# Kernel tuning notes

Measured on AMD Instinct MI355X. Metric: run time of the kernel, lower is better.

Reference implementation:

```python
import jax, jax.numpy as jnp
import numpy as np
from jax import lax

TH = 1.0      # float threshold from __init__
TAU = 0.1     # forward default
EPS_BN = 1e-5
EPS_NORM = 1e-8


def setup_inputs() -> dict:
    key = jax.random.key(0)
    ks = jax.random.split(key, 9)
    B, C, T, N = 1, 256, 128, 256
    HID = 32
    return {
        'v_rel': jax.random.normal(ks[0], (B, C, T, N), jnp.float32),
        'w1': jax.random.normal(ks[1], (HID, 2), jnp.float32) * 0.05,
        'b1': jax.random.normal(ks[2], (HID,), jnp.float32) * 0.05,
        'bn_gamma': jax.random.uniform(ks[3], (HID,), jnp.float32) + 0.5,
        'bn_beta': jax.random.normal(ks[4], (HID,), jnp.float32) * 0.05,
        'bn_mean': jax.random.normal(ks[5], (HID,), jnp.float32) * 0.05,
        'bn_var': jax.random.uniform(ks[6], (HID,), jnp.float32) + 0.5,
        'w2': jax.random.normal(ks[7], (1, HID), jnp.float32) * 0.05,
        'b2': jax.random.normal(ks[8], (1,), jnp.float32) * 0.05,
    }


def _per_ch(p):
    return p[None, :, None, None]


def _dist_mat(v_rel, w1, b1, bn_gamma, bn_beta, bn_mean, bn_var, w2, b2):
    # d_type == 'learned': pairwise diffs of last-frame absolute features (first 2 channels)
    x = v_rel[:, :2, -1, :]                       # (1, 2, N)
    d = x[:, :, :, None] - x[:, :, None, :]       # (1, 2, N, N) == reshaped temp
    h = jnp.einsum('oi,binm->bonm', w1, d) + _per_ch(b1)   # 1x1 conv -> (1, HID, N, N)
    h = jax.nn.relu(h)
    # BatchNorm2d, inference mode with running stats
    h = (h - _per_ch(bn_mean)) * (_per_ch(bn_gamma) / jnp.sqrt(_per_ch(bn_var) + EPS_BN)) + _per_ch(bn_beta)
    h = jnp.exp(jnp.einsum('oi,binm->bonm', w2, h) + _per_ch(b2))  # (1, 1, N, N)
    dm = 0.5 * (h + jnp.swapaxes(h, -1, -2))      # mean of stack(temp, temp^T)
    return dm[:, 0].mean(axis=0)                  # squeeze(1).mean(dim=0) -> (N, N)


def _find_group_indices(dist, th):
    # Serial union-find over strictly-lower-triangular close pairs in row-major
    # order, exactly matching the torch loop semantics; expressed as lax.scan.
    N = dist.shape[0]
    flat = jnp.arange(N * N)
    r = flat // N
    c = flat % N
    ok = (c < r) & (dist[r, c] <= th)

    def step(labels, inp):
        ri, ci, o = inp
        merged = jnp.where(labels == labels[ri], labels[ci], labels)
        return jnp.where(o, merged, labels), None

    labels, _ = lax.scan(step, jnp.arange(N), (r, c, ok))
    # relabel sorted-unique labels to 0..K-1 (labels are in [0, N))
    present = jnp.zeros(N, jnp.int32).at[labels].set(1)
    ranks = jnp.cumsum(present) - 1
    return ranks[labels]


def reference(v_rel, w1, b1, bn_gamma, bn_beta, bn_mean, bn_var, w2, b2):
    B, C, T, N = v_rel.shape
    dm = _dist_mat(v_rel, w1, b1, bn_gamma, bn_beta, bn_mean, bn_var, w2, b2)  # (N, N)
    group_indices = _find_group_indices(dm, TH)[None]                          # (1, N)
    # group_backprop_trick with tau=0.1, hard=True (straight-through)
    sig = jax.nn.sigmoid(-(dm - TH) / TAU)
    sig_norm = sig / (sig.sum(axis=0, keepdims=True) + EPS_NORM)
    v = v_rel[0]                                                               # (C, T, N)
    v_soft = jnp.einsum('ctn,nm->ctm', v, sig_norm)
    v_grouped = (lax.stop_gradient(v - v_soft) + v_soft)[None]                 # (1, C, T, N)
    dist_mat_full = jnp.broadcast_to(dm[None, None], (B, T, N, N))
    return v_grouped, group_indices, dist_mat_full
```

## Files before the change

### kernel.cpp

```cpp
#include <hip/hip_runtime.h>
#include <stdint.h>

#define NN 256
#define TT 128
#define CC 256
#define TH_F 1.0f
#define EPS_BN_F 1e-5f

#define OUT0_ELEMS (CC * TT * NN)
#define OUT1_OFF   OUT0_ELEMS
#define OUT2_OFF   (OUT0_ELEMS + NN)

#define N0_F4      (OUT0_ELEMS / 4)
#define NSLICE_F4  (NN * NN / 4)
#define F4_PER_BLK 1024
#define COPY0_BLKS (N0_F4 / F4_PER_BLK)
#define COPY2_BLKS (((TT - 1) * NSLICE_F4) / F4_PER_BLK)

typedef float vfloat4 __attribute__((ext_vector_type(4)));

__global__ __launch_bounds__(256) void k1_dm_out0(
        const float* __restrict__ v_rel,
        const float* __restrict__ w1,
        const float* __restrict__ b1,
        const float* __restrict__ bn_g,
        const float* __restrict__ bn_b,
        const float* __restrict__ bn_m,
        const float* __restrict__ bn_v,
        const float* __restrict__ w2,
        const float* __restrict__ b2,
        float* __restrict__ out) {
    const int tid = threadIdx.x;
    if (blockIdx.x < NN) {
        float* __restrict__ dm = out + OUT2_OFF;
        const int m = tid;
        const int n = blockIdx.x;
        const float x0n = v_rel[127 * 256 + n];
        const float x0m = v_rel[127 * 256 + m];
        const float x1n = v_rel[255 * 256 + n];
        const float x1m = v_rel[255 * 256 + m];
        const float d0 = x0n - x0m;
        const float d1 = x1n - x1m;
        float accF = 0.0f, accB = 0.0f;
        #pragma unroll
        for (int o = 0; o < 32; ++o) {
            const float w10 = w1[2 * o], w11 = w1[2 * o + 1];
            const float scale = bn_g[o] / sqrtf(bn_v[o] + EPS_BN_F);
            const float mu = bn_m[o], be = bn_b[o], bb = b1[o], a = w2[o];
            float preF = w10 * d0 + w11 * d1 + bb;
            float preB = w10 * (-d0) + w11 * (-d1) + bb;
            float hF = fmaxf(preF, 0.0f);
            float hB = fmaxf(preB, 0.0f);
            accF += a * ((hF - mu) * scale + be);
            accB += a * ((hB - mu) * scale + be);
        }
        const float sF = expf(accF + b2[0]);
        const float sB = expf(accB + b2[0]);
        dm[n * 256 + m] = 0.5f * (sF + sB);
    } else {
        const int base = (int)(blockIdx.x - NN) * F4_PER_BLK + tid;
        const vfloat4* __restrict__ in4 = reinterpret_cast<const vfloat4*>(v_rel);
        vfloat4* __restrict__ o0 = reinterpret_cast<vfloat4*>(out);
        #pragma unroll
        for (int q = 0; q < 4; ++q) {
            const int i = base + q * 256;
            __builtin_nontemporal_store(in4[i], o0 + i);
        }
    }
}

__device__ __forceinline__ uint32_t rl32(uint32_t v, uint32_t l) {
    return (uint32_t)__builtin_amdgcn_readlane((int)v, (int)l);
}
__device__ __forceinline__ uint64_t rl64(uint64_t v, uint32_t l) {
    uint32_t lo = rl32((uint32_t)v, l);
    uint32_t hi = rl32((uint32_t)(v >> 32), l);
    return ((uint64_t)hi << 32) | lo;
}

template<int NW>
__device__ __forceinline__ uint32_t pick_lab(uint32_t lab0, uint32_t lab1,
                                             uint32_t lab2, uint32_t lab3,
                                             uint32_t p) {
    const uint32_t ls = p & 63u;
    uint32_t a = rl32(lab0, ls);
    if (NW == 1) return a;
    uint32_t b = rl32(lab1, ls);
    const uint32_t g = (p >> 6) & 3u;
    if (NW == 2) return (g & 1u) ? b : a;
    uint32_t c = rl32(lab2, ls);
    uint32_t d = (NW > 3) ? rl32(lab3, ls) : c;
    uint32_t ab = (g & 1u) ? b : a;
    uint32_t cd = (g & 1u) ? d : c;
    return (g & 2u) ? cd : ab;
}

template<int NW>
__device__ __forceinline__ void scan_chunk(const int K, const int lane,
                                           uint32_t& lab0, uint32_t& lab1,
                                           uint32_t& lab2, uint32_t& lab3,
                                           uint32_t& labw,
                                           const uint64_t* __restrict__ bits,
                                           bool& fast, uint32_t& V) {
    const int base = (K * 64 + lane) * 4;
    uint64_t Wr0 = bits[base + 0];
    uint64_t Wr1 = (NW > 1) ? bits[base + 1] : 0;
    uint64_t Wr2 = (NW > 2) ? bits[base + 2] : 0;
    uint64_t Wr3 = (NW > 3) ? bits[base + 3] : 0;

    const uint64_t rowOr = Wr0 | Wr1 | Wr2 | Wr3;
    const uint64_t nonempty = __ballot(rowOr != 0);

    if (fast && nonempty == ~0ull) {
        labw = V;
        return;
    }

    for (int rr = 0; rr < 64; ++rr) {
        const bool rowEmpty = ((nonempty >> rr) & 1ull) == 0ull;
        if (fast) {
            if (!rowEmpty) {
                labw = ((uint32_t)lane == (uint32_t)rr) ? V : labw;
                continue;
            }
            fast = (V == (uint32_t)(K * 64 + rr));
            continue;
        }
        const uint64_t w0 = rl64(Wr0, (uint32_t)rr);
        const uint64_t w1 = (NW > 1) ? rl64(Wr1, (uint32_t)rr) : 0;
        const uint64_t w2 = (NW > 2) ? rl64(Wr2, (uint32_t)rr) : 0;
        const uint64_t w3 = (NW > 3) ? rl64(Wr3, (uint32_t)rr) : 0;
        uint32_t f0 = w0 ? (uint32_t)__builtin_ctzll(w0) : 512u;
        uint32_t p = f0;
        if (NW > 1) { uint32_t f = w1 ? (uint32_t)__builtin_ctzll(w1) + 64u  : 512u; p = p < f ? p : f; }
        if (NW > 2) { uint32_t f = w2 ? (uint32_t)__builtin_ctzll(w2) + 128u : 512u; p = p < f ? p : f; }
        if (NW > 3) { uint32_t f = w3 ? (uint32_t)__builtin_ctzll(w3) + 192u : 512u; p = p < f ? p : f; }
        const uint32_t lc = pick_lab<NW>(lab0, lab1, lab2, lab3, p & 255u);
        const uint32_t upd = (p < 256u) ? (uint32_t)rr : 64u;
        labw = ((uint32_t)lane == upd) ? lc : labw;
        uint32_t cur = lc;
        uint64_t R0, R1 = 0, R2 = 0, R3 = 0;
        for (;;) {
            R0 = __ballot(lab0 != cur);
            if (NW > 1) R1 = __ballot(lab1 != cur);
            if (NW > 2) R2 = __ballot(lab2 != cur);
            if (NW > 3) R3 = __ballot(lab3 != cur);
            const uint64_t Q0 = R0 & w0;
            const uint64_t Q1 = (NW > 1) ? (R1 & w1) : 0;
            const uint64_t Q2 = (NW > 2) ? (R2 & w2) : 0;
            const uint64_t Q3 = (NW > 3) ? (R3 & w3) : 0;
            if (!(Q0 | Q1 | Q2 | Q3)) break;
            uint32_t h0 = Q0 ? (uint32_t)__builtin_ctzll(Q0) : 512u;
            uint32_t p2 = h0;
            if (NW > 1) { uint32_t h = Q1 ? (uint32_t)__builtin_ctzll(Q1) + 64u  : 512u; p2 = p2 < h ? p2 : h; }
            if (NW > 2) { uint32_t h = Q2 ? (uint32_t)__builtin_ctzll(Q2) + 128u : 512u; p2 = p2 < h ? p2 : h; }
            if (NW > 3) { uint32_t h = Q3 ? (uint32_t)__builtin_ctzll(Q3) + 192u : 512u; p2 = p2 < h ? p2 : h; }
            const uint32_t lc2 = pick_lab<NW>(lab0, lab1, lab2, lab3, p2);
            lab0 = (lab0 == cur) ? lc2 : lab0;
            if (NW > 1) lab1 = (lab1 == cur) ? lc2 : lab1;
            if (NW > 2) lab2 = (lab2 == cur) ? lc2 : lab2;
            if (NW > 3) lab3 = (lab3 == cur) ? lc2 : lab3;
            cur = lc2;
        }
        const uint64_t pmK = (rr == 63) ? ~0ull : ((1ull << (rr + 1)) - 1ull);
        uint64_t nb = R0 & ((NW - 1 == 0) ? pmK : ~0ull);
        if (NW > 1) nb |= R1 & ((NW - 1 == 1) ? pmK : ~0ull);
        if (NW > 2) nb |= R2 & ((NW - 1 == 2) ? pmK : ~0ull);
        if (NW > 3) nb |= R3 & pmK;
        if (nb == 0) { fast = true; V = cur; }
    }
}

__global__ __launch_bounds__(256) void k2_scan_out2(float* __restrict__ out) {
    const int tid = threadIdx.x;
    const float* __restrict__ dm = out + OUT2_OFF;

    if (blockIdx.x == 0) {
        __shared__ __align__(16) uint64_t bits[1024];
        __shared__ uint32_t lab_arr[256];
        __shared__ uint32_t pres[256];
        __shared__ uint32_t rnk[256];

        for (int i = 0; i < 4; ++i) {
            const int wid = i * 256 + tid;
            const int r = wid >> 2;
            const int gw = wid & 3;
            uint64_t bm = 0;
            const int cbase = gw * 64;
            if (cbase < r) {
                const float4* p = reinterpret_cast<const float4*>(dm + r * 256 + cbase);
                #pragma unroll
                for (int q = 0; q < 16; ++q) {
                    const float4 v = p[q];
                    const int c0 = cbase + q * 4;
                    if (c0 + 0 < r && v.x <= TH_F) bm |= 1ull << (q * 4 + 0);
                    if (c0 + 1 < r && v.y <= TH_F) bm |= 1ull << (q * 4 + 1);
                    if (c0 + 2 < r && v.z <= TH_F) bm |= 1ull << (q * 4 + 2);
                    if (c0 + 3 < r && v.w <= TH_F) bm |= 1ull << (q * 4 + 3);
                }
            }
            bits[wid] = bm;
        }
        __syncthreads();

        if (tid < 64) {
            const int lane = tid;
            uint32_t lab0 = (uint32_t)lane;
            uint32_t lab1 = (uint32_t)(64 + lane);
            uint32_t lab2 = (uint32_t)(128 + lane);
            uint32_t lab3 = (uint32_t)(192 + lane);
            bool fast = true;
            uint32_t V = 0;

            scan_chunk<1>(0, lane, lab0, lab1, lab2, lab3, lab0, bits, fast, V);
            scan_chunk<2>(1, lane, lab0, lab1, lab2, lab3, lab1, bits, fast, V);
            scan_chunk<3>(2, lane, lab0, lab1, lab2, lab3, lab2, bits, fast, V);
            scan_chunk<4>(3, lane, lab0, lab1, lab2, lab3, lab3, bits, fast, V);

            lab_arr[lane]       = lab0;
            lab_arr[64 + lane]  = lab1;
            lab_arr[128 + lane] = lab2;
            lab_arr[192 + lane] = lab3;
        }
        __syncthreads();

        pres[tid] = 0;
        __syncthreads();
        pres[lab_arr[tid]] = 1;
        __syncthreads();
        if (tid < 64) {
            const int lane = tid;
            const int c0 = 4 * lane;
            const uint32_t t0 = pres[c0 + 0];
            const uint32_t t1 = pres[c0 + 1];
            const uint32_t t2 = pres[c0 + 2];
            const uint32_t t3 = pres[c0 + 3];
            const uint32_t s0 = t0, s1 = s0 + t1, s2 = s1 + t2, s3 = s2 + t3;
            uint32_t incl = s3;
            #pragma unroll
            for (int off = 1; off < 64; off <<= 1) {
                uint32_t u = __shfl_up(incl, off);
                if (lane >= off) incl += u;
            }
            const uint32_t excl = incl - s3;
            rnk[c0 + 0] = excl + s0 - 1;
            rnk[c0 + 1] = excl + s1 - 1;
            rnk[c0 + 2] = excl + s2 - 1;
            rnk[c0 + 3] = excl + s3 - 1;
        }
        __syncthreads();
        out[OUT1_OFF + tid] = (float)rnk[lab_arr[tid]];
    } else {
        const int j = (int)(blockIdx.x - 1) * F4_PER_BLK + tid;
        const vfloat4* __restrict__ dm4 = reinterpret_cast<const vfloat4*>(dm);
        vfloat4* __restrict__ o2 = reinterpret_cast<vfloat4*>(out + OUT2_OFF);
        #pragma unroll
        for (int q = 0; q < 4; ++q) {
            const int jj = j + q * 256;
            __builtin_nontemporal_store(dm4[jj & (NSLICE_F4 - 1)],
                                        o2 + (jj + NSLICE_F4));
        }
    }
}

extern "C" void kernel_launch(void* const* d_in, const int* in_sizes, int n_in,
                              void* d_out, int out_size, void* d_ws, size_t ws_size,
                              hipStream_t stream) {
    const float* v_rel = (const float*)d_in[0];
    const float* w1    = (const float*)d_in[1];
    const float* b1    = (const float*)d_in[2];
    const float* bn_g  = (const float*)d_in[3];
    const float* bn_b  = (const float*)d_in[4];
    const float* bn_m  = (const float*)d_in[5];
    const float* bn_v  = (const float*)d_in[6];
    const float* w2    = (const float*)d_in[7];
    const float* b2    = (const float*)d_in[8];
    float* out = (float*)d_out;

    k1_dm_out0<<<NN + COPY0_BLKS, 256, 0, stream>>>(v_rel, w1, b1, bn_g, bn_b,
                                                    bn_m, bn_v, w2, b2, out);
    k2_scan_out2<<<1 + COPY2_BLKS, 256, 0, stream>>>(out);
}
```

Baseline: 117.2 us.

## Recompute dist matrix per broadcast block and write all time slices in first kernel

The first kernel now computes distance-matrix values directly inside 1024 broadcast blocks and writes them to all 128 time slices. This removes the second kernel's read-back-and-copy of the 127 replicated slices. The second kernel becomes a single 1024-thread block that only builds the bitmask and runs the union-find scan. The cost is 16x redundant recomputation of the small MLP per element, and the serial scan kernel no longer overlaps with any copy work.

After: 150.6 us. +28.5%, slower.

```diff
diff --git a/kernel.cpp b/kernel.cpp
--- a/kernel.cpp
+++ b/kernel.cpp
@@ -12,14 +12,47 @@
 #define OUT2_OFF   (OUT0_ELEMS + NN)
 
 #define N0_F4      (OUT0_ELEMS / 4)
-#define NSLICE_F4  (NN * NN / 4)
 #define F4_PER_BLK 1024
 #define COPY0_BLKS (N0_F4 / F4_PER_BLK)
-#define COPY2_BLKS (((TT - 1) * NSLICE_F4) / F4_PER_BLK)
+#define BCAST_BLKS 1024
 
 typedef float vfloat4 __attribute__((ext_vector_type(4)));
 
-__global__ __launch_bounds__(256) void k1_dm_out0(
+__device__ __forceinline__ float dm_val(const float* __restrict__ v_rel,
+                                        const float* __restrict__ w1,
+                                        const float* __restrict__ b1,
+                                        const float* __restrict__ bn_g,
+                                        const float* __restrict__ bn_b,
+                                        const float* __restrict__ bn_m,
+                                        const float* __restrict__ bn_v,
+                                        const float* __restrict__ w2,
+                                        const float b2v,
+                                        int n, int m) {
+    const float x0n = v_rel[127 * 256 + n];
+    const float x0m = v_rel[127 * 256 + m];
+    const float x1n = v_rel[255 * 256 + n];
+    const float x1m = v_rel[255 * 256 + m];
+    const float d0 = x0n - x0m;
+    const float d1 = x1n - x1m;
+    float accF = 0.0f, accB = 0.0f;
+    #pragma unroll
+    for (int o = 0; o < 32; ++o) {
+        const float w10 = w1[2 * o], w11 = w1[2 * o + 1];
+        const float scale = bn_g[o] / sqrtf(bn_v[o] + EPS_BN_F);
+        const float mu = bn_m[o], be = bn_b[o], bb = b1[o], a = w2[o];
+        float preF = w10 * d0 + w11 * d1 + bb;
+        float preB = w10 * (-d0) + w11 * (-d1) + bb;
+        float hF = fmaxf(preF, 0.0f);
+        float hB = fmaxf(preB, 0.0f);
+        accF += a * ((hF - mu) * scale + be);
+        accB += a * ((hB - mu) * scale + be);
+    }
+    const float sF = expf(accF + b2v);
+    const float sB = expf(accB + b2v);
+    return 0.5f * (sF + sB);
+}
+
+__global__ __launch_bounds__(256) void k1_bulk(
         const float* __restrict__ v_rel,
         const float* __restrict__ w1,
         const float* __restrict__ b1,
@@ -31,40 +64,34 @@
         const float* __restrict__ b2,
         float* __restrict__ out) {
     const int tid = threadIdx.x;
-    if (blockIdx.x < NN) {
-        float* __restrict__ dm = out + OUT2_OFF;
-        const int m = tid;
-        const int n = blockIdx.x;
-        const float x0n = v_rel[127 * 256 + n];
-        const float x0m = v_rel[127 * 256 + m];
-        const float x1n = v_rel[255 * 256 + n];
-        const float x1m = v_rel[255 * 256 + m];
-        const float d0 = x0n - x0m;
-        const float d1 = x1n - x1m;
-        float accF = 0.0f, accB = 0.0f;
-        #pragma unroll
-        for (int o = 0; o < 32; ++o) {
-            const float w10 = w1[2 * o], w11 = w1[2 * o + 1];
-            const float scale = bn_g[o] / sqrtf(bn_v[o] + EPS_BN_F);
-            const float mu = bn_m[o], be = bn_b[o], bb = b1[o], a = w2[o];
-            float preF = w10 * d0 + w11 * d1 + bb;
-            float preB = w10 * (-d0) + w11 * (-d1) + bb;
-            float hF = fmaxf(preF, 0.0f);
-            float hB = fmaxf(preB, 0.0f);
-            accF += a * ((hF - mu) * scale + be);
-            accB += a * ((hB - mu) * scale + be);
-        }
-        const float sF = expf(accF + b2[0]);
-        const float sB = expf(accB + b2[0]);
-        dm[n * 256 + m] = 0.5f * (sF + sB);
-    } else {
-        const int base = (int)(blockIdx.x - NN) * F4_PER_BLK + tid;
+    if (blockIdx.x < COPY0_BLKS) {
+        const int base = (int)blockIdx.x * F4_PER_BLK + tid;
         const vfloat4* __restrict__ in4 = reinterpret_cast<const vfloat4*>(v_rel);
         vfloat4* __restrict__ o0 = reinterpret_cast<vfloat4*>(out);
         #pragma unroll
         for (int q = 0; q < 4; ++q) {
             const int i = base + q * 256;
             __builtin_nontemporal_store(in4[i], o0 + i);
+        }
+    } else {
+        const int b  = (int)blockIdx.x - COPY0_BLKS;
+        const int rg = b >> 4;
+        const int tc = b & 15;
+        const int row = rg * 4 + (tid >> 6);
+        const int m0  = (tid & 63) * 4;
+        const float b2v = b2[0];
+        vfloat4 f4;
+        f4.x = dm_val(v_rel, w1, b1, bn_g, bn_b, bn_m, bn_v, w2, b2v, row, m0 + 0);
+        f4.y = dm_val(v_rel, w1, b1, bn_g, bn_b, bn_m, bn_v, w2, b2v, row, m0 + 1);
+        f4.z = dm_val(v_rel, w1, b1, bn_g, bn_b, bn_m, bn_v, w2, b2v, row, m0 + 2);
+        f4.w = dm_val(v_rel, w1, b1, bn_g, bn_b, bn_m, bn_v, w2, b2v, row, m0 + 3);
+        float* __restrict__ o2 = out + OUT2_OFF;
+        const int off = row * 256 + m0;
+        #pragma unroll
+        for (int s = 0; s < 8; ++s) {
+            const int t = tc * 8 + s;
+            __builtin_nontemporal_store(
+                f4, reinterpret_cast<vfloat4*>(o2 + t * (NN * NN) + off));
         }
     }
 }
@@ -171,96 +198,84 @@
     }
 }
 
-__global__ __launch_bounds__(256) void k2_scan_out2(float* __restrict__ out) {
+__global__ __launch_bounds__(1024) void k2_scan(float* __restrict__ out) {
     const int tid = threadIdx.x;
     const float* __restrict__ dm = out + OUT2_OFF;
 
-    if (blockIdx.x == 0) {
-        __shared__ __align__(16) uint64_t bits[1024];
-        __shared__ uint32_t lab_arr[256];
-        __shared__ uint32_t pres[256];
-        __shared__ uint32_t rnk[256];
-
-        for (int i = 0; i < 4; ++i) {
-            const int wid = i * 256 + tid;
-            const int r = wid >> 2;
-            const int gw = wid & 3;
-            uint64_t bm = 0;
-            const int cbase = gw * 64;
-            if (cbase < r) {
-                const float4* p = reinterpret_cast<const float4*>(dm + r * 256 + cbase);
-                #pragma unroll
-                for (int q = 0; q < 16; ++q) {
-                    const float4 v = p[q];
-                    const int c0 = cbase + q * 4;
-                    if (c0 + 0 < r && v.x <= TH_F) bm |= 1ull << (q * 4 + 0);
-                    if (c0 + 1 < r && v.y <= TH_F) bm |= 1ull << (q * 4 + 1);
-                    if (c0 + 2 < r && v.z <= TH_F) bm |= 1ull << (q * 4 + 2);
-                    if (c0 + 3 < r && v.w <= TH_F) bm |= 1ull << (q * 4 + 3);
-                }
+    __shared__ __align__(16) uint64_t bits[1024];
+    __shared__ uint32_t lab_arr[256];
+    __shared__ uint32_t pres[256];
+    __shared__ uint32_t rnk[256];
+
+    {
+        const int wid = tid;
+        const int r = wid >> 2;
+        const int gw = wid & 3;
+        uint64_t bm = 0;
+        const int cbase = gw * 64;
+        if (cbase < r) {
+            const float4* p = reinterpret_cast<const float4*>(dm + r * 256 + cbase);
+            #pragma unroll
+            for (int q = 0; q < 16; ++q) {
+                const float4 v = p[q];
+                const int c0 = cbase + q * 4;
+                if (c0 + 0 < r && v.x <= TH_F) bm |= 1ull << (q * 4 + 0);
+                if (c0 + 1 < r && v.y <= TH_F) bm |= 1ull << (q * 4 + 1);
+                if (c0 + 2 < r && v.z <= TH_F) bm |= 1ull << (q * 4 + 2);
+                if (c0 + 3 < r && v.w <= TH_F) bm |= 1ull << (q * 4 + 3);
             }
-            bits[wid] = bm;
-        }
-        __syncthreads();
-
-        if (tid < 64) {
-            const int lane = tid;
-            uint32_t lab0 = (uint32_t)lane;
-            uint32_t lab1 = (uint32_t)(64 + lane);
-            uint32_t lab2 = (uint32_t)(128 + lane);
-            uint32_t lab3 = (uint32_t)(192 + lane);
-            bool fast = true;
-            uint32_t V = 0;
-
-            scan_chunk<1>(0, lane, lab0, lab1, lab2, lab3, lab0, bits, fast, V);
-            scan_chunk<2>(1, lane, lab0, lab1, lab2, lab3, lab1, bits, fast, V);
-            scan_chunk<3>(2, lane, lab0, lab1, lab2, lab3, lab2, bits, fast, V);
-            scan_chunk<4>(3, lane, lab0, lab1, lab2, lab3, lab3, bits, fast, V);
-
-            lab_arr[lane]       = lab0;
-            lab_arr[64 + lane]  = lab1;
-            lab_arr[128 + lane] = lab2;
-            lab_arr[192 + lane] = lab3;
-        }
-        __syncthreads();
-
-        pres[tid] = 0;
-        __syncthreads();
-        pres[lab_arr[tid]] = 1;
-        __syncthreads();
-        if (tid < 64) {
-            const int lane = tid;
-            const int c0 = 4 * lane;
-            const uint32_t t0 = pres[c0 + 0];
-            const uint32_t t1 = pres[c0 + 1];
-            const uint32_t t2 = pres[c0 + 2];
-            const uint32_t t3 = pres[c0 + 3];
-            const uint32_t s0 = t0, s1 = s0 + t1, s2 = s1 + t2, s3 = s2 + t3;
-            uint32_t incl = s3;
-            #pragma unroll
-            for (int off = 1; off < 64; off <<= 1) {
-                uint32_t u = __shfl_up(incl, off);
-                if (lane >= off) incl += u;
-            }
-            const uint32_t excl = incl - s3;
-            rnk[c0 + 0] = excl + s0 - 1;
-            rnk[c0 + 1] = excl + s1 - 1;
-            rnk[c0 + 2] = excl + s2 - 1;
-            rnk[c0 + 3] = excl + s3 - 1;
-        }
-        __syncthreads();
-        out[OUT1_OFF + tid] = (float)rnk[lab_arr[tid]];
-    } else {
-        const int j = (int)(blockIdx.x - 1) * F4_PER_BLK + tid;
-        const vfloat4* __restrict__ dm4 = reinterpret_cast<const vfloat4*>(dm);
-        vfloat4* __restrict__ o2 = reinterpret_cast<vfloat4*>(out + OUT2_OFF);
+        }
+        bits[wid] = bm;
+    }
+    __syncthreads();
+
+    if (tid < 64) {
+        const int lane = tid;
+        uint32_t lab0 = (uint32_t)lane;
+        uint32_t lab1 = (uint32_t)(64 + lane);
+        uint32_t lab2 = (uint32_t)(128 + lane);
+        uint32_t lab3 = (uint32_t)(192 + lane);
+        bool fast = true;
+        uint32_t V = 0;
+
+        scan_chunk<1>(0, lane, lab0, lab1, lab2, lab3, lab0, bits, fast, V);
+        scan_chunk<2>(1, lane, lab0, lab1, lab2, lab3, lab1, bits, fast, V);
+        scan_chunk<3>(2, lane, lab0, lab1, lab2, lab3, lab2, bits, fast, V);
+        scan_chunk<4>(3, lane, lab0, lab1, lab2, lab3, lab3, bits, fast, V);
+
+        lab_arr[lane]       = lab0;
+        lab_arr[64 + lane]  = lab1;
+        lab_arr[128 + lane] = lab2;
+        lab_arr[192 + lane] = lab3;
+    }
+    __syncthreads();
+
+    if (tid < 256) pres[tid] = 0;
+    __syncthreads();
+    if (tid < 256) pres[lab_arr[tid]] = 1;
+    __syncthreads();
+    if (tid < 64) {
+        const int lane = tid;
+        const int c0 = 4 * lane;
+        const uint32_t t0 = pres[c0 + 0];
+        const uint32_t t1 = pres[c0 + 1];
+        const uint32_t t2 = pres[c0 + 2];
+        const uint32_t t3 = pres[c0 + 3];
+        const uint32_t s0 = t0, s1 = s0 + t1, s2 = s1 + t2, s3 = s2 + t3;
+        uint32_t incl = s3;
         #pragma unroll
-        for (int q = 0; q < 4; ++q) {
-            const int jj = j + q * 256;
-            __builtin_nontemporal_store(dm4[jj & (NSLICE_F4 - 1)],
-                                        o2 + (jj + NSLICE_F4));
-        }
-    }
+        for (int off = 1; off < 64; off <<= 1) {
+            uint32_t u = __shfl_up(incl, off);
+            if (lane >= off) incl += u;
+        }
+        const uint32_t excl = incl - s3;
+        rnk[c0 + 0] = excl + s0 - 1;
+        rnk[c0 + 1] = excl + s1 - 1;
+        rnk[c0 + 2] = excl + s2 - 1;
+        rnk[c0 + 3] = excl + s3 - 1;
+    }
+    __syncthreads();
+    if (tid < 256) out[OUT1_OFF + tid] = (float)rnk[lab_arr[tid]];
 }
 
 extern "C" void kernel_launch(void* const* d_in, const int* in_sizes, int n_in,
@@ -277,7 +292,8 @@
     const float* b2    = (const float*)d_in[8];
     float* out = (float*)d_out;
 
-    k1_dm_out0<<<NN + COPY0_BLKS, 256, 0, stream>>>(v_rel, w1, b1, bn_g, bn_b,
-                                                    bn_m, bn_v, w2, b2, out);
-    k2_scan_out2<<<1 + COPY2_BLKS, 256, 0, stream>>>(out);
-}
+    k1_bulk<<<COPY0_BLKS + BCAST_BLKS, 256, 0, stream>>>(v_rel, w1, b1, bn_g,
+                                                         bn_b, bn_m, bn_v, w2,
+                                                         b2, out);
+    k2_scan<<<1, 1024, 0, stream>>>(out);
+}
```

## Fuse dm, copy and scan kernels into persistent grid with atomic barrier

Applied to the files above, without the earlier changes.

Merges the two kernels into one 1024-block persistent kernel. The first 256 blocks compute the distance matrix and bump an atomic counter, every block copies v_rel to output 0, and then all blocks spin until the counter shows the matrix is complete. Block 0 then runs the union-find scan while the rest broadcast the matrix into output 2 with a grid-stride loop. The aim is to overlap the serial scan with the big copies and remove the kernel boundary. In exchange it adds a counter-init launch and relies on every block being co-resident; the counter is kept in the last element of output 2, which the broadcast later overwrites.

Result: slower. 227.2 us (+93.8%).

```diff
diff --git a/kernel.cpp b/kernel.cpp
--- a/kernel.cpp
+++ b/kernel.cpp
@@ -10,63 +10,19 @@
 #define OUT0_ELEMS (CC * TT * NN)
 #define OUT1_OFF   OUT0_ELEMS
 #define OUT2_OFF   (OUT0_ELEMS + NN)
+#define OUT2_ELEMS (TT * NN * NN)
 
 #define N0_F4      (OUT0_ELEMS / 4)
 #define NSLICE_F4  (NN * NN / 4)
-#define F4_PER_BLK 1024
-#define COPY0_BLKS (N0_F4 / F4_PER_BLK)
-#define COPY2_BLKS (((TT - 1) * NSLICE_F4) / F4_PER_BLK)
+#define GRID_BLKS  1024
+#define CHUNK_F4   1024
+#define OUT2_CHUNKS (((TT - 1) * NSLICE_F4) / CHUNK_F4)
 
 typedef float vfloat4 __attribute__((ext_vector_type(4)));
 
-__global__ __launch_bounds__(256) void k1_dm_out0(
-        const float* __restrict__ v_rel,
-        const float* __restrict__ w1,
-        const float* __restrict__ b1,
-        const float* __restrict__ bn_g,
-        const float* __restrict__ bn_b,
-        const float* __restrict__ bn_m,
-        const float* __restrict__ bn_v,
-        const float* __restrict__ w2,
-        const float* __restrict__ b2,
-        float* __restrict__ out) {
-    const int tid = threadIdx.x;
-    if (blockIdx.x < NN) {
-        float* __restrict__ dm = out + OUT2_OFF;
-        const int m = tid;
-        const int n = blockIdx.x;
-        const float x0n = v_rel[127 * 256 + n];
-        const float x0m = v_rel[127 * 256 + m];
-        const float x1n = v_rel[255 * 256 + n];
-        const float x1m = v_rel[255 * 256 + m];
-        const float d0 = x0n - x0m;
-        const float d1 = x1n - x1m;
-        float accF = 0.0f, accB = 0.0f;
-        #pragma unroll
-        for (int o = 0; o < 32; ++o) {
-            const float w10 = w1[2 * o], w11 = w1[2 * o + 1];
-            const float scale = bn_g[o] / sqrtf(bn_v[o] + EPS_BN_F);
-            const float mu = bn_m[o], be = bn_b[o], bb = b1[o], a = w2[o];
-            float preF = w10 * d0 + w11 * d1 + bb;
-            float preB = w10 * (-d0) + w11 * (-d1) + bb;
-            float hF = fmaxf(preF, 0.0f);
-            float hB = fmaxf(preB, 0.0f);
-            accF += a * ((hF - mu) * scale + be);
-            accB += a * ((hB - mu) * scale + be);
-        }
-        const float sF = expf(accF + b2[0]);
-        const float sB = expf(accB + b2[0]);
-        dm[n * 256 + m] = 0.5f * (sF + sB);
-    } else {
-        const int base = (int)(blockIdx.x - NN) * F4_PER_BLK + tid;
-        const vfloat4* __restrict__ in4 = reinterpret_cast<const vfloat4*>(v_rel);
-        vfloat4* __restrict__ o0 = reinterpret_cast<vfloat4*>(out);
-        #pragma unroll
-        for (int q = 0; q < 4; ++q) {
-            const int i = base + q * 256;
-            __builtin_nontemporal_store(in4[i], o0 + i);
-        }
-    }
+__global__ void init_cnt(float* __restrict__ out) {
+    if (threadIdx.x == 0)
+        *(uint32_t*)(out + OUT2_OFF + OUT2_ELEMS - 1) = 0u;
 }
 
 __device__ __forceinline__ uint32_t rl32(uint32_t v, uint32_t l) {
@@ -171,16 +127,80 @@
     }
 }
 
-__global__ __launch_bounds__(256) void k2_scan_out2(float* __restrict__ out) {
+__global__ __launch_bounds__(256, 4) void fused(
+        const float* __restrict__ v_rel,
+        const float* __restrict__ w1,
+        const float* __restrict__ b1,
+        const float* __restrict__ bn_g,
+        const float* __restrict__ bn_b,
+        const float* __restrict__ bn_m,
+        const float* __restrict__ bn_v,
+        const float* __restrict__ w2,
+        const float* __restrict__ b2,
+        float* __restrict__ out) {
     const int tid = threadIdx.x;
-    const float* __restrict__ dm = out + OUT2_OFF;
-
-    if (blockIdx.x == 0) {
-        __shared__ __align__(16) uint64_t bits[1024];
-        __shared__ uint32_t lab_arr[256];
-        __shared__ uint32_t pres[256];
-        __shared__ uint32_t rnk[256];
-
+    const int bid = blockIdx.x;
+    float* __restrict__ dm = out + OUT2_OFF;
+    uint32_t* cnt = (uint32_t*)(out + OUT2_OFF + OUT2_ELEMS - 1);
+
+    __shared__ __align__(16) uint64_t bits[1024];
+    __shared__ uint32_t lab_arr[256];
+    __shared__ uint32_t pres[256];
+    __shared__ uint32_t rnk[256];
+
+    if (bid < NN) {
+        const int m = tid;
+        const int n = bid;
+        const float x0n = v_rel[127 * 256 + n];
+        const float x0m = v_rel[127 * 256 + m];
+        const float x1n = v_rel[255 * 256 + n];
+        const float x1m = v_rel[255 * 256 + m];
+        const float d0 = x0n - x0m;
+        const float d1 = x1n - x1m;
+        float accF = 0.0f, accB = 0.0f;
+        #pragma unroll
+        for (int o = 0; o < 32; ++o) {
+            const float w10 = w1[2 * o], w11 = w1[2 * o + 1];
+            const float scale = bn_g[o] / sqrtf(bn_v[o] + EPS_BN_F);
+            const float mu = bn_m[o], be = bn_b[o], bb = b1[o], a = w2[o];
+            float preF = w10 * d0 + w11 * d1 + bb;
+            float preB = w10 * (-d0) + w11 * (-d1) + bb;
+            float hF = fmaxf(preF, 0.0f);
+            float hB = fmaxf(preB, 0.0f);
+            accF += a * ((hF - mu) * scale + be);
+            accB += a * ((hB - mu) * scale + be);
+        }
+        const float sF = expf(accF + b2[0]);
+        const float sB = expf(accB + b2[0]);
+        dm[n * 256 + m] = 0.5f * (sF + sB);
+        __threadfence();
+        __syncthreads();
+        if (tid == 0) atomicAdd(cnt, 1u);
+    }
+
+    {
+        const vfloat4* __restrict__ in4 = reinterpret_cast<const vfloat4*>(v_rel);
+        vfloat4* __restrict__ o0 = reinterpret_cast<vfloat4*>(out);
+        #pragma unroll
+        for (int h = 0; h < 2; ++h) {
+            const int base = (bid + h * GRID_BLKS) * CHUNK_F4 + tid;
+            #pragma unroll
+            for (int q = 0; q < 4; ++q) {
+                const int i = base + q * 256;
+                __builtin_nontemporal_store(in4[i], o0 + i);
+            }
+        }
+    }
+
+    if (tid == 0) {
+        while (__hip_atomic_load(cnt, __ATOMIC_ACQUIRE,
+                                 __HIP_MEMORY_SCOPE_AGENT) < (uint32_t)NN) {
+        }
+    }
+    __syncthreads();
+    __threadfence();
+
+    if (bid == 0) {
         for (int i = 0; i < 4; ++i) {
             const int wid = i * 256 + tid;
             const int r = wid >> 2;
@@ -251,14 +271,16 @@
         __syncthreads();
         out[OUT1_OFF + tid] = (float)rnk[lab_arr[tid]];
     } else {
-        const int j = (int)(blockIdx.x - 1) * F4_PER_BLK + tid;
         const vfloat4* __restrict__ dm4 = reinterpret_cast<const vfloat4*>(dm);
         vfloat4* __restrict__ o2 = reinterpret_cast<vfloat4*>(out + OUT2_OFF);
-        #pragma unroll
-        for (int q = 0; q < 4; ++q) {
-            const int jj = j + q * 256;
-            __builtin_nontemporal_store(dm4[jj & (NSLICE_F4 - 1)],
-                                        o2 + (jj + NSLICE_F4));
+        for (int c = bid - 1; c < OUT2_CHUNKS; c += GRID_BLKS - 1) {
+            const int j = c * CHUNK_F4 + tid;
+            #pragma unroll
+            for (int q = 0; q < 4; ++q) {
+                const int jj = j + q * 256;
+                __builtin_nontemporal_store(dm4[jj & (NSLICE_F4 - 1)],
+                                            o2 + (jj + NSLICE_F4));
+            }
         }
     }
 }
@@ -277,7 +299,7 @@
     const float* b2    = (const float*)d_in[8];
     float* out = (float*)d_out;
 
-    k1_dm_out0<<<NN + COPY0_BLKS, 256, 0, stream>>>(v_rel, w1, b1, bn_g, bn_b,
-                                                    bn_m, bn_v, w2, b2, out);
-    k2_scan_out2<<<1 + COPY2_BLKS, 256, 0, stream>>>(out);
-}
+    init_cnt<<<1, 64, 0, stream>>>(out);
+    fused<<<GRID_BLKS, 256, 0, stream>>>(v_rel, w1, b1, bn_g, bn_b, bn_m,
+                                         bn_v, w2, b2, out);
+}
```

## Broadcast dist-matrix rows to all T slices inside the first kernel

Applied to the files above, without the earlier changes.

Each dist-matrix block now stages its computed row in shared memory and writes it straight to all 128 time slices of the broadcast output. The second kernel shrinks to a single block that only runs the union-find scan. This removes the re-read of the distance matrix and moves the 32 MB broadcast write off the second launch, where it ran concurrently with the serial scan, into the first kernel alongside the v_rel copy. The 256 distance blocks now each write 128 rows, so the work between blocks becomes less even.

Result: no change. 117.7 us (+0.4%).

```diff
diff --git a/kernel.cpp b/kernel.cpp
--- a/kernel.cpp
+++ b/kernel.cpp
@@ -12,14 +12,12 @@
 #define OUT2_OFF   (OUT0_ELEMS + NN)
 
 #define N0_F4      (OUT0_ELEMS / 4)
-#define NSLICE_F4  (NN * NN / 4)
-#define F4_PER_BLK 1024
-#define COPY0_BLKS (N0_F4 / F4_PER_BLK)
-#define COPY2_BLKS (((TT - 1) * NSLICE_F4) / F4_PER_BLK)
+#define CHUNK_F4   1024
+#define COPY0_BLKS (N0_F4 / CHUNK_F4)
 
 typedef float vfloat4 __attribute__((ext_vector_type(4)));
 
-__global__ __launch_bounds__(256) void k1_dm_out0(
+__global__ __launch_bounds__(256) void k1_bulk(
         const float* __restrict__ v_rel,
         const float* __restrict__ w1,
         const float* __restrict__ b1,
@@ -31,10 +29,12 @@
         const float* __restrict__ b2,
         float* __restrict__ out) {
     const int tid = threadIdx.x;
-    if (blockIdx.x < NN) {
-        float* __restrict__ dm = out + OUT2_OFF;
+    const int bid = blockIdx.x;
+
+    if (bid < NN) {
+        __shared__ float row[256];
         const int m = tid;
-        const int n = blockIdx.x;
+        const int n = bid;
         const float x0n = v_rel[127 * 256 + n];
         const float x0m = v_rel[127 * 256 + m];
         const float x1n = v_rel[255 * 256 + n];
@@ -56,9 +56,20 @@
         }
         const float sF = expf(accF + b2[0]);
         const float sB = expf(accB + b2[0]);
-        dm[n * 256 + m] = 0.5f * (sF + sB);
+        const float val = 0.5f * (sF + sB);
+
+        float* __restrict__ o2 = out + OUT2_OFF;
+        o2[n * 256 + m] = val;
+        row[m] = val;
+        __syncthreads();
+        const vfloat4 v4 = *reinterpret_cast<const vfloat4*>(&row[(tid & 63) * 4]);
+        const int f4i = tid & 63;
+        for (int t = 1 + (tid >> 6); t < TT; t += 4) {
+            vfloat4* dst = reinterpret_cast<vfloat4*>(o2 + t * (NN * NN) + n * 256);
+            __builtin_nontemporal_store(v4, dst + f4i);
+        }
     } else {
-        const int base = (int)(blockIdx.x - NN) * F4_PER_BLK + tid;
+        const int base = (bid - NN) * CHUNK_F4 + tid;
         const vfloat4* __restrict__ in4 = reinterpret_cast<const vfloat4*>(v_rel);
         vfloat4* __restrict__ o0 = reinterpret_cast<vfloat4*>(out);
         #pragma unroll
@@ -171,96 +182,84 @@
     }
 }
 
-__global__ __launch_bounds__(256) void k2_scan_out2(float* __restrict__ out) {
+__global__ __launch_bounds__(256) void k2_scan(float* __restrict__ out) {
     const int tid = threadIdx.x;
     const float* __restrict__ dm = out + OUT2_OFF;
 
-    if (blockIdx.x == 0) {
-        __shared__ __align__(16) uint64_t bits[1024];
-        __shared__ uint32_t lab_arr[256];
-        __shared__ uint32_t pres[256];
-        __shared__ uint32_t rnk[256];
-
-        for (int i = 0; i < 4; ++i) {
-            const int wid = i * 256 + tid;
-            const int r = wid >> 2;
-            const int gw = wid & 3;
-            uint64_t bm = 0;
-            const int cbase = gw * 64;
-            if (cbase < r) {
-                const float4* p = reinterpret_cast<const float4*>(dm + r * 256 + cbase);
-                #pragma unroll
-                for (int q = 0; q < 16; ++q) {
-                    const float4 v = p[q];
-                    const int c0 = cbase + q * 4;
-                    if (c0 + 0 < r && v.x <= TH_F) bm |= 1ull << (q * 4 + 0);
-                    if (c0 + 1 < r && v.y <= TH_F) bm |= 1ull << (q * 4 + 1);
-                    if (c0 + 2 < r && v.z <= TH_F) bm |= 1ull << (q * 4 + 2);
-                    if (c0 + 3 < r && v.w <= TH_F) bm |= 1ull << (q * 4 + 3);
-                }
+    __shared__ __align__(16) uint64_t bits[1024];
+    __shared__ uint32_t lab_arr[256];
+    __shared__ uint32_t pres[256];
+    __shared__ uint32_t rnk[256];
+
+    for (int i = 0; i < 4; ++i) {
+        const int wid = i * 256 + tid;
+        const int r = wid >> 2;
+        const int gw = wid & 3;
+        uint64_t bm = 0;
+        const int cbase = gw * 64;
+        if (cbase < r) {
+            const float4* p = reinterpret_cast<const float4*>(dm + r * 256 + cbase);
+            #pragma unroll
+            for (int q = 0; q < 16; ++q) {
+                const float4 v = p[q];
+                const int c0 = cbase + q * 4;
+                if (c0 + 0 < r && v.x <= TH_F) bm |= 1ull << (q * 4 + 0);
+                if (c0 + 1 < r && v.y <= TH_F) bm |= 1ull << (q * 4 + 1);
+                if (c0 + 2 < r && v.z <= TH_F) bm |= 1ull << (q * 4 + 2);
+                if (c0 + 3 < r && v.w <= TH_F) bm |= 1ull << (q * 4 + 3);
             }
-            bits[wid] = bm;
-        }
-        __syncthreads();
-
-        if (tid < 64) {
-            const int lane = tid;
-            uint32_t lab0 = (uint32_t)lane;
-            uint32_t lab1 = (uint32_t)(64 + lane);
-            uint32_t lab2 = (uint32_t)(128 + lane);
-            uint32_t lab3 = (uint32_t)(192 + lane);
-            bool fast = true;
-            uint32_t V = 0;
-
-            scan_chunk<1>(0, lane, lab0, lab1, lab2, lab3, lab0, bits, fast, V);
-            scan_chunk<2>(1, lane, lab0, lab1, lab2, lab3, lab1, bits, fast, V);
-            scan_chunk<3>(2, lane, lab0, lab1, lab2, lab3, lab2, bits, fast, V);
-            scan_chunk<4>(3, lane, lab0, lab1, lab2, lab3, lab3, bits, fast, V);
-
-            lab_arr[lane]       = lab0;
-            lab_arr[64 + lane]  = lab1;
-            lab_arr[128 + lane] = lab2;
-            lab_arr[192 + lane] = lab3;
-        }
-        __syncthreads();
-
-        pres[tid] = 0;
-        __syncthreads();
-        pres[lab_arr[tid]] = 1;
-        __syncthreads();
-        if (tid < 64) {
-            const int lane = tid;
-            const int c0 = 4 * lane;
-            const uint32_t t0 = pres[c0 + 0];
-            const uint32_t t1 = pres[c0 + 1];
-            const uint32_t t2 = pres[c0 + 2];
-            const uint32_t t3 = pres[c0 + 3];
-            const uint32_t s0 = t0, s1 = s0 + t1, s2 = s1 + t2, s3 = s2 + t3;
-            uint32_t incl = s3;
-            #pragma unroll
-            for (int off = 1; off < 64; off <<= 1) {
-                uint32_t u = __shfl_up(incl, off);
-                if (lane >= off) incl += u;
-            }
-            const uint32_t excl = incl - s3;
-            rnk[c0 + 0] = excl + s0 - 1;
-            rnk[c0 + 1] = excl + s1 - 1;
-            rnk[c0 + 2] = excl + s2 - 1;
-            rnk[c0 + 3] = excl + s3 - 1;
-        }
-        __syncthreads();
-        out[OUT1_OFF + tid] = (float)rnk[lab_arr[tid]];
-    } else {
-        const int j = (int)(blockIdx.x - 1) * F4_PER_BLK + tid;
-        const vfloat4* __restrict__ dm4 = reinterpret_cast<const vfloat4*>(dm);
-        vfloat4* __restrict__ o2 = reinterpret_cast<vfloat4*>(out + OUT2_OFF);
+        }
+        bits[wid] = bm;
+    }
+    __syncthreads();
+
+    if (tid < 64) {
+        const int lane = tid;
+        uint32_t lab0 = (uint32_t)lane;
+        uint32_t lab1 = (uint32_t)(64 + lane);
+        uint32_t lab2 = (uint32_t)(128 + lane);
+        uint32_t lab3 = (uint32_t)(192 + lane);
+        bool fast = true;
+        uint32_t V = 0;
+
+        scan_chunk<1>(0, lane, lab0, lab1, lab2, lab3, lab0, bits, fast, V);
+        scan_chunk<2>(1, lane, lab0, lab1, lab2, lab3, lab1, bits, fast, V);
+        scan_chunk<3>(2, lane, lab0, lab1, lab2, lab3, lab2, bits, fast, V);
+        scan_chunk<4>(3, lane, lab0, lab1, lab2, lab3, lab3, bits, fast, V);
+
+        lab_arr[lane]       = lab0;
+        lab_arr[64 + lane]  = lab1;
+        lab_arr[128 + lane] = lab2;
+        lab_arr[192 + lane] = lab3;
+    }
+    __syncthreads();
+
+    pres[tid] = 0;
+    __syncthreads();
+    pres[lab_arr[tid]] = 1;
+    __syncthreads();
+    if (tid < 64) {
+        const int lane = tid;
+        const int c0 = 4 * lane;
+        const uint32_t t0 = pres[c0 + 0];
+        const uint32_t t1 = pres[c0 + 1];
+        const uint32_t t2 = pres[c0 + 2];
+        const uint32_t t3 = pres[c0 + 3];
+        const uint32_t s0 = t0, s1 = s0 + t1, s2 = s1 + t2, s3 = s2 + t3;
+        uint32_t incl = s3;
         #pragma unroll
-        for (int q = 0; q < 4; ++q) {
-            const int jj = j + q * 256;
-            __builtin_nontemporal_store(dm4[jj & (NSLICE_F4 - 1)],
-                                        o2 + (jj + NSLICE_F4));
-        }
-    }
+        for (int off = 1; off < 64; off <<= 1) {
+            uint32_t u = __shfl_up(incl, off);
+            if (lane >= off) incl += u;
+        }
+        const uint32_t excl = incl - s3;
+        rnk[c0 + 0] = excl + s0 - 1;
+        rnk[c0 + 1] = excl + s1 - 1;
+        rnk[c0 + 2] = excl + s2 - 1;
+        rnk[c0 + 3] = excl + s3 - 1;
+    }
+    __syncthreads();
+    out[OUT1_OFF + tid] = (float)rnk[lab_arr[tid]];
 }
 
 extern "C" void kernel_launch(void* const* d_in, const int* in_sizes, int n_in,
@@ -277,7 +276,7 @@
     const float* b2    = (const float*)d_in[8];
     float* out = (float*)d_out;
 
-    k1_dm_out0<<<NN + COPY0_BLKS, 256, 0, stream>>>(v_rel, w1, b1, bn_g, bn_b,
-                                                    bn_m, bn_v, w2, b2, out);
-    k2_scan_out2<<<1 + COPY2_BLKS, 256, 0, stream>>>(out);
-}
+    k1_bulk<<<NN + COPY0_BLKS, 256, 0, stream>>>(v_rel, w1, b1, bn_g, bn_b,
+                                                 bn_m, bn_v, w2, b2, out);
+    k2_scan<<<1, 256, 0, stream>>>(out);
+}
```
